# Kernel tuning notes

Hardware: AMD Instinct MI355X
Metric: run time of the kernel (lower is better)

Reference implementation:

```python
import jax, jax.numpy as jnp
import numpy as np

N, E, D, C, G = 100000, 3200000, 128, 10, 512
BN_EPS = 1e-5


def setup_inputs() -> dict:
    key = jax.random.key(0)
    ks = jax.random.split(key, 16)
    s = 0.05
    return {
        "x": jax.random.normal(ks[0], (N, D), jnp.float32),
        "edge_index": jax.random.randint(ks[1], (2, E), 0, N, dtype=jnp.int64),
        "batch": jnp.sort(jax.random.randint(ks[2], (N,), 0, G, dtype=jnp.int64)),
        # 5 stacked GINConv MLPs: Linear->ReLU->Linear->ReLU->BatchNorm
        "conv_W1": jax.random.normal(ks[3], (5, D, D), jnp.float32) * s,
        "conv_b1": jnp.zeros((5, D), jnp.float32),
        "conv_W2": jax.random.normal(ks[4], (5, D, D), jnp.float32) * s,
        "conv_b2": jnp.zeros((5, D), jnp.float32),
        "conv_gamma": jnp.ones((5, D), jnp.float32),
        "conv_beta": jnp.zeros((5, D), jnp.float32),
        # fc1 / fc2: Linear->ReLU->BatchNorm (fc2 is SHARED across stages)
        "fc1_W": jax.random.normal(ks[5], (D, D), jnp.float32) * s,
        "fc1_b": jnp.zeros((D,), jnp.float32),
        "fc1_gamma": jnp.ones((D,), jnp.float32),
        "fc1_beta": jnp.zeros((D,), jnp.float32),
        "fc2_W": jax.random.normal(ks[6], (D, D), jnp.float32) * s,
        "fc2_b": jnp.zeros((D,), jnp.float32),
        "fc2_gamma": jnp.ones((D,), jnp.float32),
        "fc2_beta": jnp.zeros((D,), jnp.float32),
        "lin_W": jax.random.normal(ks[7], (D, C), jnp.float32) * s,
        "lin_b": jnp.zeros((C,), jnp.float32),
    }


def _bn(h, gamma, beta):
    # training-mode BatchNorm1d: batch stats, biased variance
    m = h.mean(axis=0)
    v = h.var(axis=0)
    return (h - m) * jax.lax.rsqrt(v + BN_EPS) * gamma + beta


def _fc(h, W, b, gamma, beta):
    return _bn(jax.nn.relu(h @ W + b), gamma, beta)


def reference(x, edge_index, batch, conv_W1, conv_b1, conv_W2, conv_b2,
              conv_gamma, conv_beta, fc1_W, fc1_b, fc1_gamma, fc1_beta,
              fc2_W, fc2_b, fc2_gamma, fc2_beta, lin_W, lin_b):
    src, dst = edge_index[0], edge_index[1]
    pool = lambda h: jax.ops.segment_sum(h, batch, num_segments=G)

    g = _fc(pool(x), fc1_W, fc1_b, fc1_gamma, fc1_beta)  # x0_g
    total = g
    h = x
    for i in range(5):
        # GINConv, eps=0: nn((1+eps)*x + sum_{j in N(i)} x_j)
        agg = jax.ops.segment_sum(h[src], dst, num_segments=N)
        z = h + agg
        z = jax.nn.relu(z @ conv_W1[i] + conv_b1[i])
        z = jax.nn.relu(z @ conv_W2[i] + conv_b2[i])
        h = _bn(z, conv_gamma[i], conv_beta[i])
        g = _fc(g + pool(h), fc2_W, fc2_b, fc2_gamma, fc2_beta)
        total = total + g
    # dropout omitted (inference); final classifier
    logits = total @ lin_W + lin_b
    return jax.nn.log_softmax(logits, axis=-1)
```

## Files before the change

kernel.cpp:

```cpp
#include <hip/hip_runtime.h>
#include <hip/hip_bf16.h>
#include <math.h>

#define D 128
#define NG 512
#define NC 10
#define PAD 96
#define CAP 704
#define BN_EPS 1e-5f

typedef __attribute__((ext_vector_type(8))) short frag_ab;
typedef __attribute__((ext_vector_type(4))) float f32x4;

__device__ __forceinline__ ushort f2bf(float v) {
    __hip_bfloat16 h = __float2bfloat16(v);
    union { __hip_bfloat16 h; ushort u; } c;
    c.h = h;
    return c.u;
}
__device__ __forceinline__ float bflo(uint u) { return __uint_as_float(u << 16); }
__device__ __forceinline__ float bfhi(uint u) { return __uint_as_float(u & 0xffff0000u); }
__device__ __forceinline__ uint packbf(float x, float y) {
    return (uint)f2bf(x) | ((uint)f2bf(y) << 16);
}

__global__ void zero_ints(int* __restrict__ p, int n) {
    int i = blockIdx.x * blockDim.x + threadIdx.x;
    int s = gridDim.x * blockDim.x;
    for (; i < n; i += s) p[i] = 0;
}

__global__ void scatter_bucket(const int* __restrict__ srcs, const int* __restrict__ dsts, int E,
                               int* __restrict__ bcnt, uint* __restrict__ ebuf) {
    int i = blockIdx.x * blockDim.x + threadIdx.x;
    int s = gridDim.x * blockDim.x;
    for (; i < E; i += s) {
        int d = dsts[i];
        int b = d >> 4;
        int pos = atomicAdd(&bcnt[b], 1);
        if (pos < CAP) ebuf[(size_t)b * CAP + pos] = (uint)srcs[i] | ((uint)(d & 15) << 24);
    }
}

__global__ void csr_phaseB(const uint* __restrict__ ebuf, const int* __restrict__ bcnt,
                           int* __restrict__ cnt, int* __restrict__ pad, int N) {
    int b = blockIdx.x;
    int tid = threadIdx.x;
    int n0 = b << 4;
    __shared__ int lcur[16];
    __shared__ int lcnt2[16];
    __shared__ int lpad[16 * PAD];
    if (tid < 16) lcur[tid] = tid * PAD;
    __syncthreads();
    int ec = bcnt[b];
    if (ec > CAP) ec = CAP;
    const uint* eb = ebuf + (size_t)b * CAP;
    for (int e = tid; e < ec; e += 256) {
        uint w = eb[e];
        int ld = w >> 24;
        int pos = atomicAdd(&lcur[ld], 1);
        if (pos < ld * PAD + PAD) lpad[pos] = (int)(w & 0x00FFFFFFu);
    }
    __syncthreads();
    int ne = N - n0;
    if (ne > 16) ne = 16;
    if (tid < 16) {
        int c = lcur[tid] - tid * PAD;
        if (c > PAD) c = PAD;
        lcnt2[tid] = c;
    }
    __syncthreads();
    if (tid < ne) cnt[n0 + tid] = lcnt2[tid];
    const int CH = PAD / 4;
    int4* dst4 = (int4*)(pad + (size_t)n0 * PAD);
    const int4* s4 = (const int4*)lpad;
    for (int i = tid; i < 16 * CH; i += 256) {
        int node = i / CH, ch = i - node * CH;
        if (node < ne && ch * 4 < lcnt2[node]) dst4[node * CH + ch] = s4[node * CH + ch];
    }
}

__global__ void gstart_bsearch(const int* __restrict__ batch, int N, int* __restrict__ gstart) {
    int g = blockIdx.x * blockDim.x + threadIdx.x;
    if (g > NG) return;
    if (g == NG) { gstart[NG] = N; return; }
    int lo = 0, hi = N;
    while (lo < hi) {
        int mid = (lo + hi) >> 1;
        if (batch[mid] < g) lo = mid + 1; else hi = mid;
    }
    gstart[g] = lo;
}

__global__ void cvt_bf16(const float* __restrict__ in, uint* __restrict__ out, int nPairs) {
    int i = blockIdx.x * blockDim.x + threadIdx.x;
    int s = gridDim.x * blockDim.x;
    const float2* in2 = (const float2*)in;
    for (; i < nPairs; i += s) {
        float2 v = in2[i];
        out[i] = packbf(v.x, v.y);
    }
}

__global__ void prep_w(const float* __restrict__ W1, const float* __restrict__ W2,
                       ushort* __restrict__ Wt) {
    int m = blockIdx.x;
    const float* W = (m < 5) ? (W1 + (size_t)m * D * D) : (W2 + (size_t)(m - 5) * D * D);
    ushort* out = Wt + (size_t)m * D * D;
    __shared__ ushort ws[D * D];
    int tid = threadIdx.x;
    for (int i = tid; i < D * D; i += 256) ws[i] = f2bf(W[i]);
    __syncthreads();
    int n = tid >> 1, kh = (tid & 1) << 6;
    uint* op = (uint*)(out + n * D + kh);
#pragma unroll 8
    for (int j = 0; j < 32; ++j) {
        uint lo = ws[(kh + 2 * j) * D + n];
        uint hi = ws[(kh + 2 * j + 1) * D + n];
        op[j] = lo | (hi << 16);
    }
}

#define ACC8(V) { s0 += bflo(V.x); s1 += bfhi(V.x); s2 += bflo(V.y); s3 += bfhi(V.y); \
                  s4 += bflo(V.z); s5 += bfhi(V.z); s6 += bflo(V.w); s7 += bfhi(V.w); }

__global__ void agg_pad(const uint4* __restrict__ src4, const float* __restrict__ stats,
                        const float* __restrict__ gamma, const float* __restrict__ beta,
                        float invN, const int* __restrict__ deg, const int* __restrict__ pad,
                        uint4* __restrict__ out4, int N) {
    int gtid = blockIdx.x * blockDim.x + threadIdx.x;
    int grp = gtid >> 4;
    int c16 = gtid & 15;
    int ng = (gridDim.x * blockDim.x) >> 4;
    int cb = c16 * 8;
    float A[8], B[8];
#pragma unroll
    for (int j = 0; j < 8; ++j) { A[j] = 1.f; B[j] = 0.f; }
    if (stats) {
#pragma unroll
        for (int j = 0; j < 8; ++j) {
            int c = cb + j;
            float m = stats[c] * invN;
            float v = fmaxf(stats[D + c] * invN - m * m, 0.f);
            float r = rsqrtf(v + BN_EPS);
            A[j] = r * gamma[c];
            B[j] = beta[c] - m * A[j];
        }
    }
    for (int n = grp; n < N; n += ng) {
        float s0 = 0.f, s1 = 0.f, s2 = 0.f, s3 = 0.f, s4 = 0.f, s5 = 0.f, s6 = 0.f, s7 = 0.f;
        {
            uint4 v = src4[(size_t)n * 16 + c16];
            ACC8(v);
        }
        const int* cp = pad + (size_t)n * PAD;
        int dg = deg[n];
        if (dg > PAD) dg = PAD;
        int e = 0;
        for (; e + 8 <= dg; e += 8) {
            int i0 = cp[e], i1 = cp[e + 1], i2 = cp[e + 2], i3 = cp[e + 3];
            int i4 = cp[e + 4], i5 = cp[e + 5], i6 = cp[e + 6], i7 = cp[e + 7];
            uint4 v0 = src4[(size_t)i0 * 16 + c16];
            uint4 v1 = src4[(size_t)i1 * 16 + c16];
            uint4 v2 = src4[(size_t)i2 * 16 + c16];
            uint4 v3 = src4[(size_t)i3 * 16 + c16];
            uint4 v4 = src4[(size_t)i4 * 16 + c16];
            uint4 v5 = src4[(size_t)i5 * 16 + c16];
            uint4 v6 = src4[(size_t)i6 * 16 + c16];
            uint4 v7 = src4[(size_t)i7 * 16 + c16];
            ACC8(v0); ACC8(v1); ACC8(v2); ACC8(v3);
            ACC8(v4); ACC8(v5); ACC8(v6); ACC8(v7);
        }
        for (; e < dg; ++e) {
            uint4 v0 = src4[(size_t)cp[e] * 16 + c16];
            ACC8(v0);
        }
        float db = (float)(dg + 1);
        uint4 o;
        o.x = packbf(s0 * A[0] + db * B[0], s1 * A[1] + db * B[1]);
        o.y = packbf(s2 * A[2] + db * B[2], s3 * A[3] + db * B[3]);
        o.z = packbf(s4 * A[4] + db * B[4], s5 * A[5] + db * B[5]);
        o.w = packbf(s6 * A[6] + db * B[6], s7 * A[7] + db * B[7]);
        out4[(size_t)n * 16 + c16] = o;
    }
}

__launch_bounds__(256, 2)
__global__ void gin_mlp(const uint* __restrict__ z, const ushort* __restrict__ w1t,
                        const float* __restrict__ b1, const ushort* __restrict__ w2t,
                        const float* __restrict__ b2, uint* __restrict__ outp, int N) {
    int tid = threadIdx.x;
    int lane = tid & 63;
    int wv = tid >> 6;
    int col = lane & 15;
    int kq = lane >> 4;
    int blk = blockIdx.x;
    int m0 = blk * 64 + wv * 16;
    __shared__ __align__(16) ushort cs[64 * D];

    int arow = m0 + col;
    if (arow >= N) arow = N - 1;
    const char* zrow = (const char*)z + (size_t)arow * 256 + kq * 16;
    frag_ab a0 = *(const frag_ab*)(zrow);
    frag_ab a1 = *(const frag_ab*)(zrow + 64);
    frag_ab a2 = *(const frag_ab*)(zrow + 128);
    frag_ab a3 = *(const frag_ab*)(zrow + 192);

    f32x4 acc[8];
#pragma unroll
    for (int n = 0; n < 8; ++n) {
        float bz = b1[n * 16 + col];
        acc[n] = (f32x4){bz, bz, bz, bz};
    }
    const char* wl1 = (const char*)w1t + (size_t)col * 256 + kq * 16;
#pragma unroll
    for (int kc = 0; kc < 4; ++kc) {
        frag_ab av = (kc == 0) ? a0 : (kc == 1) ? a1 : (kc == 2) ? a2 : a3;
#pragma unroll
        for (int n = 0; n < 8; ++n) {
            frag_ab bv = *(const frag_ab*)(wl1 + n * 4096 + kc * 64);
            acc[n] = __builtin_amdgcn_mfma_f32_16x16x32_bf16(av, bv, acc[n], 0, 0, 0);
        }
    }
    int rbase = wv * 16 + kq * 4;
#pragma unroll
    for (int n = 0; n < 8; ++n) {
#pragma unroll
        for (int r = 0; r < 4; ++r) {
            int row = rbase + r;
            int colo = n * 16 + col;
            int chunk = (colo >> 3) ^ (row & 15);
            cs[row * D + chunk * 8 + (colo & 7)] = f2bf(fmaxf(acc[n][r], 0.f));
        }
    }
    __syncthreads();

    int lrow = wv * 16 + col;
    frag_ab c0, c1, c2, c3;
    c0 = *(const frag_ab*)(cs + lrow * D + (((0 << 2) + kq) ^ col) * 8);
    c1 = *(const frag_ab*)(cs + lrow * D + (((1 << 2) + kq) ^ col) * 8);
    c2 = *(const frag_ab*)(cs + lrow * D + (((2 << 2) + kq) ^ col) * 8);
    c3 = *(const frag_ab*)(cs + lrow * D + (((3 << 2) + kq) ^ col) * 8);

#pragma unroll
    for (int n = 0; n < 8; ++n) {
        float bz = b2[n * 16 + col];
        acc[n] = (f32x4){bz, bz, bz, bz};
    }
    const char* wl2 = (const char*)w2t + (size_t)col * 256 + kq * 16;
#pragma unroll
    for (int kc = 0; kc < 4; ++kc) {
        frag_ab av = (kc == 0) ? c0 : (kc == 1) ? c1 : (kc == 2) ? c2 : c3;
#pragma unroll
        for (int n = 0; n < 8; ++n) {
            frag_ab bv = *(const frag_ab*)(wl2 + n * 4096 + kc * 64);
            acc[n] = __builtin_amdgcn_mfma_f32_16x16x32_bf16(av, bv, acc[n], 0, 0, 0);
        }
    }
    __syncthreads();

#pragma unroll
    for (int n = 0; n < 8; ++n) {
#pragma unroll
        for (int r = 0; r < 4; ++r) {
            int row = rbase + r;
            int colo = n * 16 + col;
            int chunk = (colo >> 3) ^ (row & 15);
            cs[row * D + chunk * 8 + (colo & 7)] = f2bf(fmaxf(acc[n][r], 0.f));
        }
    }
    __syncthreads();

    const uint4* csv = (const uint4*)cs;
    uint4* og = (uint4*)outp;
#pragma unroll
    for (int p = 0; p < 4; ++p) {
        int idx = p * 256 + tid;
        int row = idx >> 4;
        int j = idx & 15;
        uint4 v = csv[row * 16 + (j ^ (row & 15))];
        if (blk * 64 + row < N) og[(size_t)blk * 1024 + idx] = v;
    }
}

template <int BF16>
__global__ void pool_stats(const void* __restrict__ zptr, const int* __restrict__ gstart,
                           float* __restrict__ pool, float* __restrict__ sq) {
    int g = blockIdx.x;
    int tid = threadIdx.x;
    int r0 = gstart[g], r1 = gstart[g + 1];
    __shared__ float red[256];
    if (BF16) {
        const uint* z = (const uint*)zptr;
        int uc = tid & 63;
        int qq = tid >> 6;
        float s0 = 0.f, s1 = 0.f, q0 = 0.f, q1 = 0.f;
        for (int r = r0 + qq; r < r1; r += 4) {
            uint u = z[(size_t)r * 64 + uc];
            float lo = bflo(u), hi = bfhi(u);
            s0 += lo; s1 += hi;
            q0 += lo * lo; q1 += hi * hi;
        }
        float S0 = 0.f, S1 = 0.f, Q0 = 0.f, Q1 = 0.f;
        red[tid] = s0; __syncthreads();
        if (qq == 0) S0 = red[uc] + red[uc + 64] + red[uc + 128] + red[uc + 192];
        __syncthreads();
        red[tid] = s1; __syncthreads();
        if (qq == 0) S1 = red[uc] + red[uc + 64] + red[uc + 128] + red[uc + 192];
        __syncthreads();
        red[tid] = q0; __syncthreads();
        if (qq == 0) Q0 = red[uc] + red[uc + 64] + red[uc + 128] + red[uc + 192];
        __syncthreads();
        red[tid] = q1; __syncthreads();
        if (qq == 0) Q1 = red[uc] + red[uc + 64] + red[uc + 128] + red[uc + 192];
        if (qq == 0) {
            pool[g * D + 2 * uc] = S0;
            pool[g * D + 2 * uc + 1] = S1;
            sq[g * D + 2 * uc] = Q0;
            sq[g * D + 2 * uc + 1] = Q1;
        }
    } else {
        const float* z = (const float*)zptr;
        int col = tid & 127;
        int half = tid >> 7;
        float s = 0.f;
        for (int r = r0 + half; r < r1; r += 2) s += z[(size_t)r * D + col];
        red[tid] = s;
        __syncthreads();
        if (half == 0) pool[g * D + col] = red[tid] + red[tid + 128];
    }
}

__global__ void col_stats(const float* __restrict__ pool, const float* __restrict__ sq,
                          float* __restrict__ stats) {
    int c = blockIdx.x;
    int tid = threadIdx.x;
    float s = pool[tid * D + c] + pool[(tid + 256) * D + c];
    float q = sq[tid * D + c] + sq[(tid + 256) * D + c];
    __shared__ float rs[256], rq[256];
    rs[tid] = s; rq[tid] = q;
    __syncthreads();
    for (int off = 128; off > 0; off >>= 1) {
        if (tid < off) { rs[tid] += rs[tid + off]; rq[tid] += rq[tid + off]; }
        __syncthreads();
    }
    if (tid == 0) { stats[c] = rs[0]; stats[D + c] = rq[0]; }
}

__global__ void fc_forward(const float* __restrict__ pool, const float* __restrict__ stats,
                           const float* __restrict__ gamma, const float* __restrict__ beta,
                           float invN, const int* __restrict__ gstart, const float* __restrict__ gprev,
                           const float* __restrict__ W, const float* __restrict__ bias,
                           float* __restrict__ y) {
    int g = blockIdx.x;
    int tid = threadIdx.x;
    __shared__ float u[D];
    float pv = pool[g * D + tid];
    float uv;
    if (stats) {
        float m = stats[tid] * invN;
        float var = fmaxf(stats[D + tid] * invN - m * m, 0.f);
        float rs = rsqrtf(var + BN_EPS);
        float a = rs * gamma[tid];
        float b = beta[tid] - m * a;
        float cntg = (float)(gstart[g + 1] - gstart[g]);
        uv = gprev[g * D + tid] + pv * a + cntg * b;
    } else {
        uv = pv;
    }
    u[tid] = uv;
    __syncthreads();
    float acc = bias[tid];
#pragma unroll 8
    for (int k = 0; k < D; ++k) acc = fmaf(u[k], W[k * D + tid], acc);
    y[g * D + tid] = fmaxf(acc, 0.f);
}

__global__ void fc_bn2(const float* __restrict__ y, const float* __restrict__ gamma,
                       const float* __restrict__ beta, float* __restrict__ gbuf,
                       float* __restrict__ total, int first) {
    int col = blockIdx.x;
    int tid = threadIdx.x;
    int i0 = tid * D + col, i1 = (tid + 256) * D + col;
    float v0 = y[i0], v1 = y[i1];
    __shared__ float rs[256], rq[256];
    rs[tid] = v0 + v1;
    rq[tid] = v0 * v0 + v1 * v1;
    __syncthreads();
    for (int off = 128; off > 0; off >>= 1) {
        if (tid < off) { rs[tid] += rs[tid + off]; rq[tid] += rq[tid + off]; }
        __syncthreads();
    }
    __shared__ float ab[2];
    if (tid == 0) {
        const float invG = 1.f / NG;
        float m = rs[0] * invG;
        float var = fmaxf(rq[0] * invG - m * m, 0.f);
        float a = rsqrtf(var + BN_EPS) * gamma[col];
        ab[0] = a;
        ab[1] = beta[col] - m * a;
    }
    __syncthreads();
    float a = ab[0], b = ab[1];
    float g0 = v0 * a + b, g1 = v1 * a + b;
    gbuf[i0] = g0;
    gbuf[i1] = g1;
    if (first) { total[i0] = g0; total[i1] = g1; }
    else { total[i0] += g0; total[i1] += g1; }
}

__global__ void final_logits(const float* __restrict__ total, const float* __restrict__ linW,
                             const float* __restrict__ linb, float* __restrict__ out) {
    int g = blockIdx.x;
    int tid = threadIdx.x;
    __shared__ float t[D];
    __shared__ float lg[12];
    t[tid] = total[g * D + tid];
    __syncthreads();
    if (tid < NC) {
        float a = linb[tid];
        for (int k = 0; k < D; ++k) a = fmaf(t[k], linW[k * NC + tid], a);
        lg[tid] = a;
    }
    __syncthreads();
    if (tid == 0) {
        float mx = lg[0];
        for (int c = 1; c < NC; ++c) mx = fmaxf(mx, lg[c]);
        float se = 0.f;
        for (int c = 0; c < NC; ++c) se += expf(lg[c] - mx);
        lg[10] = mx + logf(se);
    }
    __syncthreads();
    if (tid < NC) out[g * NC + tid] = lg[tid] - lg[10];
}

extern "C" void kernel_launch(void* const* d_in, const int* in_sizes, int n_in,
                              void* d_out, int out_size, void* d_ws, size_t ws_size,
                              hipStream_t stream) {
    const float* x = (const float*)d_in[0];
    const int* edge = (const int*)d_in[1];
    const int* batch = (const int*)d_in[2];
    const float* convW1 = (const float*)d_in[3];
    const float* convb1 = (const float*)d_in[4];
    const float* convW2 = (const float*)d_in[5];
    const float* convb2 = (const float*)d_in[6];
    const float* convgamma = (const float*)d_in[7];
    const float* convbeta = (const float*)d_in[8];
    const float* fc1W = (const float*)d_in[9];
    const float* fc1b = (const float*)d_in[10];
    const float* fc1gamma = (const float*)d_in[11];
    const float* fc1beta = (const float*)d_in[12];
    const float* fc2W = (const float*)d_in[13];
    const float* fc2b = (const float*)d_in[14];
    const float* fc2gamma = (const float*)d_in[15];
    const float* fc2beta = (const float*)d_in[16];
    const float* linW = (const float*)d_in[17];
    const float* linb = (const float*)d_in[18];

    const int N = in_sizes[0] / D;
    const int E = in_sizes[1] / 2;
    const int* srcs = edge;
    const int* dsts = edge + E;
    const float invN = 1.f / (float)N;
    const int NBUK = (N + 15) >> 4;

    char* p = (char*)d_ws;
    auto alloc = [&](size_t bytes) -> void* {
        void* r = (void*)p;
        p += (bytes + 255) & ~(size_t)255;
        return r;
    };
    uint* xb = (uint*)alloc((size_t)N * 64 * 4);
    uint* z  = (uint*)alloc((size_t)N * 64 * 4);
    uint* zB = (uint*)alloc((size_t)N * 64 * 4);
    ushort* wt = (ushort*)alloc((size_t)10 * D * D * 2);
    int* pad = (int*)alloc((size_t)N * PAD * 4);
    int* cnt = (int*)alloc((size_t)N * 4);
    int* gstart = (int*)alloc((size_t)(NG + 1) * 4);
    int* bcnt = (int*)alloc((size_t)NBUK * 4);
    float* stats_all = (float*)alloc((size_t)5 * 2 * D * 4);
    float* pool = (float*)alloc((size_t)NG * D * 4);
    float* sqbuf = (float*)alloc((size_t)NG * D * 4);
    float* ybuf = (float*)alloc((size_t)NG * D * 4);
    float* gbuf = (float*)alloc((size_t)NG * D * 4);
    float* total = (float*)alloc((size_t)NG * D * 4);

    uint* ebuf = z;

    zero_ints<<<(NBUK + 255) / 256, 256, 0, stream>>>(bcnt, NBUK);
    gstart_bsearch<<<3, 256, 0, stream>>>(batch, N, gstart);
    scatter_bucket<<<2048, 256, 0, stream>>>(srcs, dsts, E, bcnt, ebuf);
    cvt_bf16<<<2048, 256, 0, stream>>>(x, xb, N * 64);
    prep_w<<<10, 256, 0, stream>>>(convW1, convW2, wt);
    csr_phaseB<<<NBUK, 256, 0, stream>>>(ebuf, bcnt, cnt, pad, N);

    pool_stats<0><<<NG, 256, 0, stream>>>(x, gstart, pool, nullptr);
    fc_forward<<<NG, D, 0, stream>>>(pool, nullptr, nullptr, nullptr, 0.f, nullptr, nullptr,
                                     fc1W, fc1b, ybuf);
    fc_bn2<<<D, 256, 0, stream>>>(ybuf, fc1gamma, fc1beta, gbuf, total, 1);

    const uint* src = xb;
    const int mlp_grid = (N + 63) / 64;
    for (int i = 0; i < 5; ++i) {
        const float* st = (i == 0) ? nullptr : (stats_all + (size_t)(i - 1) * 2 * D);
        const float* ga = (i == 0) ? nullptr : (convgamma + (size_t)(i - 1) * D);
        const float* be = (i == 0) ? nullptr : (convbeta + (size_t)(i - 1) * D);
        agg_pad<<<2048, 256, 0, stream>>>((const uint4*)src, st, ga, be, invN,
                                          cnt, pad, (uint4*)z, N);
        gin_mlp<<<mlp_grid, 256, 0, stream>>>(z, wt + (size_t)i * D * D, convb1 + (size_t)i * D,
                                              wt + (size_t)(5 + i) * D * D, convb2 + (size_t)i * D,
                                              zB, N);
        float* st_i = stats_all + (size_t)i * 2 * D;
        pool_stats<1><<<NG, 256, 0, stream>>>(zB, gstart, pool, sqbuf);
        col_stats<<<D, 256, 0, stream>>>(pool, sqbuf, st_i);
        fc_forward<<<NG, D, 0, stream>>>(pool, st_i,
                                         convgamma + (size_t)i * D, convbeta + (size_t)i * D,
                                         invN, gstart, gbuf, fc2W, fc2b, ybuf);
        fc_bn2<<<D, 256, 0, stream>>>(ybuf, fc2gamma, fc2beta, gbuf, total, 0);
        src = zB;
    }

    final_logits<<<NG, D, 0, stream>>>(total, linW, linb, (float*)d_out);
}
```

Before: 1.392 ms.

## Fuse neighbor aggregation into GIN MLP kernel via shared-memory tile

The padded-CSR gather-aggregate (with the previous layer's BatchNorm folded in) now runs inside the MLP kernel. Each 64-row block aggregates its rows into a swizzled LDS tile and then feeds it straight to the MFMA stages. This drops the write and re-read of the intermediate z buffer and one kernel launch per layer. Output buffers ping-pong because the source and destination can no longer alias. The cost is a fixed 64-row grid with launch bounds of 2, which may reduce the latency hiding the gather had under the old grid-stride launch.

```diff
diff --git a/kernel.cpp b/kernel.cpp
--- a/kernel.cpp
+++ b/kernel.cpp
@@ -124,87 +124,92 @@
 #define ACC8(V) { s0 += bflo(V.x); s1 += bfhi(V.x); s2 += bflo(V.y); s3 += bfhi(V.y); \
                   s4 += bflo(V.z); s5 += bfhi(V.z); s6 += bflo(V.w); s7 += bfhi(V.w); }
 
-__global__ void agg_pad(const uint4* __restrict__ src4, const float* __restrict__ stats,
-                        const float* __restrict__ gamma, const float* __restrict__ beta,
-                        float invN, const int* __restrict__ deg, const int* __restrict__ pad,
-                        uint4* __restrict__ out4, int N) {
-    int gtid = blockIdx.x * blockDim.x + threadIdx.x;
-    int grp = gtid >> 4;
-    int c16 = gtid & 15;
-    int ng = (gridDim.x * blockDim.x) >> 4;
-    int cb = c16 * 8;
-    float A[8], B[8];
-#pragma unroll
-    for (int j = 0; j < 8; ++j) { A[j] = 1.f; B[j] = 0.f; }
-    if (stats) {
-#pragma unroll
-        for (int j = 0; j < 8; ++j) {
-            int c = cb + j;
-            float m = stats[c] * invN;
-            float v = fmaxf(stats[D + c] * invN - m * m, 0.f);
-            float r = rsqrtf(v + BN_EPS);
-            A[j] = r * gamma[c];
-            B[j] = beta[c] - m * A[j];
-        }
-    }
-    for (int n = grp; n < N; n += ng) {
-        float s0 = 0.f, s1 = 0.f, s2 = 0.f, s3 = 0.f, s4 = 0.f, s5 = 0.f, s6 = 0.f, s7 = 0.f;
-        {
-            uint4 v = src4[(size_t)n * 16 + c16];
-            ACC8(v);
-        }
-        const int* cp = pad + (size_t)n * PAD;
-        int dg = deg[n];
-        if (dg > PAD) dg = PAD;
-        int e = 0;
-        for (; e + 8 <= dg; e += 8) {
-            int i0 = cp[e], i1 = cp[e + 1], i2 = cp[e + 2], i3 = cp[e + 3];
-            int i4 = cp[e + 4], i5 = cp[e + 5], i6 = cp[e + 6], i7 = cp[e + 7];
-            uint4 v0 = src4[(size_t)i0 * 16 + c16];
-            uint4 v1 = src4[(size_t)i1 * 16 + c16];
-            uint4 v2 = src4[(size_t)i2 * 16 + c16];
-            uint4 v3 = src4[(size_t)i3 * 16 + c16];
-            uint4 v4 = src4[(size_t)i4 * 16 + c16];
-            uint4 v5 = src4[(size_t)i5 * 16 + c16];
-            uint4 v6 = src4[(size_t)i6 * 16 + c16];
-            uint4 v7 = src4[(size_t)i7 * 16 + c16];
-            ACC8(v0); ACC8(v1); ACC8(v2); ACC8(v3);
-            ACC8(v4); ACC8(v5); ACC8(v6); ACC8(v7);
-        }
-        for (; e < dg; ++e) {
-            uint4 v0 = src4[(size_t)cp[e] * 16 + c16];
-            ACC8(v0);
-        }
-        float db = (float)(dg + 1);
-        uint4 o;
-        o.x = packbf(s0 * A[0] + db * B[0], s1 * A[1] + db * B[1]);
-        o.y = packbf(s2 * A[2] + db * B[2], s3 * A[3] + db * B[3]);
-        o.z = packbf(s4 * A[4] + db * B[4], s5 * A[5] + db * B[5]);
-        o.w = packbf(s6 * A[6] + db * B[6], s7 * A[7] + db * B[7]);
-        out4[(size_t)n * 16 + c16] = o;
-    }
-}
-
 __launch_bounds__(256, 2)
-__global__ void gin_mlp(const uint* __restrict__ z, const ushort* __restrict__ w1t,
-                        const float* __restrict__ b1, const ushort* __restrict__ w2t,
-                        const float* __restrict__ b2, uint* __restrict__ outp, int N) {
-    int tid = threadIdx.x;
+__global__ void gin_fused(const uint4* __restrict__ src4, const float* __restrict__ stats,
+                          const float* __restrict__ gamma, const float* __restrict__ beta,
+                          float invN, const int* __restrict__ deg, const int* __restrict__ pad,
+                          const ushort* __restrict__ w1t, const float* __restrict__ b1,
+                          const ushort* __restrict__ w2t, const float* __restrict__ b2,
+                          uint* __restrict__ outp, int N) {
+    int tid = threadIdx.x;
+    int blk = blockIdx.x;
+    int m0 = blk * 64;
+    __shared__ __align__(16) uint4 zt4[64 * 16];
+    __shared__ __align__(16) ushort cs[64 * D];
+
+    {
+        int grp = tid >> 4;
+        int c16 = tid & 15;
+        int cb = c16 * 8;
+        float A[8], B[8];
+#pragma unroll
+        for (int j = 0; j < 8; ++j) { A[j] = 1.f; B[j] = 0.f; }
+        if (stats) {
+#pragma unroll
+            for (int j = 0; j < 8; ++j) {
+                int c = cb + j;
+                float m = stats[c] * invN;
+                float v = fmaxf(stats[D + c] * invN - m * m, 0.f);
+                float r = rsqrtf(v + BN_EPS);
+                A[j] = r * gamma[c];
+                B[j] = beta[c] - m * A[j];
+            }
+        }
+#pragma unroll
+        for (int p = 0; p < 4; ++p) {
+            int lr = p * 16 + grp;
+            int n = m0 + lr;
+            uint4 o = {0u, 0u, 0u, 0u};
+            if (n < N) {
+                float s0 = 0.f, s1 = 0.f, s2 = 0.f, s3 = 0.f, s4 = 0.f, s5 = 0.f, s6 = 0.f, s7 = 0.f;
+                {
+                    uint4 v = src4[(size_t)n * 16 + c16];
+                    ACC8(v);
+                }
+                const int* cp = pad + (size_t)n * PAD;
+                int dg = deg[n];
+                if (dg > PAD) dg = PAD;
+                int e = 0;
+                for (; e + 8 <= dg; e += 8) {
+                    int i0 = cp[e], i1 = cp[e + 1], i2 = cp[e + 2], i3 = cp[e + 3];
+                    int i4 = cp[e + 4], i5 = cp[e + 5], i6 = cp[e + 6], i7 = cp[e + 7];
+                    uint4 v0 = src4[(size_t)i0 * 16 + c16];
+                    uint4 v1 = src4[(size_t)i1 * 16 + c16];
+                    uint4 v2 = src4[(size_t)i2 * 16 + c16];
+                    uint4 v3 = src4[(size_t)i3 * 16 + c16];
+                    uint4 v4 = src4[(size_t)i4 * 16 + c16];
+                    uint4 v5 = src4[(size_t)i5 * 16 + c16];
+                    uint4 v6 = src4[(size_t)i6 * 16 + c16];
+                    uint4 v7 = src4[(size_t)i7 * 16 + c16];
+                    ACC8(v0); ACC8(v1); ACC8(v2); ACC8(v3);
+                    ACC8(v4); ACC8(v5); ACC8(v6); ACC8(v7);
+                }
+                for (; e < dg; ++e) {
+                    uint4 v0 = src4[(size_t)cp[e] * 16 + c16];
+                    ACC8(v0);
+                }
+                float db = (float)(dg + 1);
+                o.x = packbf(s0 * A[0] + db * B[0], s1 * A[1] + db * B[1]);
+                o.y = packbf(s2 * A[2] + db * B[2], s3 * A[3] + db * B[3]);
+                o.z = packbf(s4 * A[4] + db * B[4], s5 * A[5] + db * B[5]);
+                o.w = packbf(s6 * A[6] + db * B[6], s7 * A[7] + db * B[7]);
+            }
+            zt4[lr * 16 + (c16 ^ (lr & 15))] = o;
+        }
+    }
+    __syncthreads();
+
     int lane = tid & 63;
     int wv = tid >> 6;
     int col = lane & 15;
     int kq = lane >> 4;
-    int blk = blockIdx.x;
-    int m0 = blk * 64 + wv * 16;
-    __shared__ __align__(16) ushort cs[64 * D];
-
-    int arow = m0 + col;
-    if (arow >= N) arow = N - 1;
-    const char* zrow = (const char*)z + (size_t)arow * 256 + kq * 16;
-    frag_ab a0 = *(const frag_ab*)(zrow);
-    frag_ab a1 = *(const frag_ab*)(zrow + 64);
-    frag_ab a2 = *(const frag_ab*)(zrow + 128);
-    frag_ab a3 = *(const frag_ab*)(zrow + 192);
+    int lrow = wv * 16 + col;
+    const ushort* ztc = (const ushort*)zt4;
+
+    frag_ab a0 = *(const frag_ab*)(ztc + lrow * D + (((0 << 2) + kq) ^ col) * 8);
+    frag_ab a1 = *(const frag_ab*)(ztc + lrow * D + (((1 << 2) + kq) ^ col) * 8);
+    frag_ab a2 = *(const frag_ab*)(ztc + lrow * D + (((2 << 2) + kq) ^ col) * 8);
+    frag_ab a3 = *(const frag_ab*)(ztc + lrow * D + (((3 << 2) + kq) ^ col) * 8);
 
     f32x4 acc[8];
 #pragma unroll
@@ -235,12 +240,10 @@
     }
     __syncthreads();
 
-    int lrow = wv * 16 + col;
-    frag_ab c0, c1, c2, c3;
-    c0 = *(const frag_ab*)(cs + lrow * D + (((0 << 2) + kq) ^ col) * 8);
-    c1 = *(const frag_ab*)(cs + lrow * D + (((1 << 2) + kq) ^ col) * 8);
-    c2 = *(const frag_ab*)(cs + lrow * D + (((2 << 2) + kq) ^ col) * 8);
-    c3 = *(const frag_ab*)(cs + lrow * D + (((3 << 2) + kq) ^ col) * 8);
+    frag_ab c0 = *(const frag_ab*)(cs + lrow * D + (((0 << 2) + kq) ^ col) * 8);
+    frag_ab c1 = *(const frag_ab*)(cs + lrow * D + (((1 << 2) + kq) ^ col) * 8);
+    frag_ab c2 = *(const frag_ab*)(cs + lrow * D + (((2 << 2) + kq) ^ col) * 8);
+    frag_ab c3 = *(const frag_ab*)(cs + lrow * D + (((3 << 2) + kq) ^ col) * 8);
 
 #pragma unroll
     for (int n = 0; n < 8; ++n) {
@@ -279,7 +282,7 @@
         int row = idx >> 4;
         int j = idx & 15;
         uint4 v = csv[row * 16 + (j ^ (row & 15))];
-        if (blk * 64 + row < N) og[(size_t)blk * 1024 + idx] = v;
+        if (m0 + row < N) og[(size_t)blk * 1024 + idx] = v;
     }
 }
 
@@ -471,7 +474,7 @@
         return r;
     };
     uint* xb = (uint*)alloc((size_t)N * 64 * 4);
-    uint* z  = (uint*)alloc((size_t)N * 64 * 4);
+    uint* zA = (uint*)alloc((size_t)N * 64 * 4);
     uint* zB = (uint*)alloc((size_t)N * 64 * 4);
     ushort* wt = (ushort*)alloc((size_t)10 * D * D * 2);
     int* pad = (int*)alloc((size_t)N * PAD * 4);
@@ -485,7 +488,7 @@
     float* gbuf = (float*)alloc((size_t)NG * D * 4);
     float* total = (float*)alloc((size_t)NG * D * 4);
 
-    uint* ebuf = z;
+    uint* ebuf = zB;
 
     zero_ints<<<(NBUK + 255) / 256, 256, 0, stream>>>(bcnt, NBUK);
     gstart_bsearch<<<3, 256, 0, stream>>>(batch, N, gstart);
@@ -500,24 +503,25 @@
     fc_bn2<<<D, 256, 0, stream>>>(ybuf, fc1gamma, fc1beta, gbuf, total, 1);
 
     const uint* src = xb;
-    const int mlp_grid = (N + 63) / 64;
+    uint* dst = zA;
+    const int fgrid = (N + 63) / 64;
     for (int i = 0; i < 5; ++i) {
         const float* st = (i == 0) ? nullptr : (stats_all + (size_t)(i - 1) * 2 * D);
         const float* ga = (i == 0) ? nullptr : (convgamma + (size_t)(i - 1) * D);
         const float* be = (i == 0) ? nullptr : (convbeta + (size_t)(i - 1) * D);
-        agg_pad<<<2048, 256, 0, stream>>>((const uint4*)src, st, ga, be, invN,
-                                          cnt, pad, (uint4*)z, N);
-        gin_mlp<<<mlp_grid, 256, 0, stream>>>(z, wt + (size_t)i * D * D, convb1 + (size_t)i * D,
-                                              wt + (size_t)(5 + i) * D * D, convb2 + (size_t)i * D,
-                                              zB, N);
+        gin_fused<<<fgrid, 256, 0, stream>>>((const uint4*)src, st, ga, be, invN, cnt, pad,
+                                             wt + (size_t)i * D * D, convb1 + (size_t)i * D,
+                                             wt + (size_t)(5 + i) * D * D, convb2 + (size_t)i * D,
+                                             dst, N);
         float* st_i = stats_all + (size_t)i * 2 * D;
-        pool_stats<1><<<NG, 256, 0, stream>>>(zB, gstart, pool, sqbuf);
+        pool_stats<1><<<NG, 256, 0, stream>>>(dst, gstart, pool, sqbuf);
         col_stats<<<D, 256, 0, stream>>>(pool, sqbuf, st_i);
         fc_forward<<<NG, D, 0, stream>>>(pool, st_i,
                                          convgamma + (size_t)i * D, convbeta + (size_t)i * D,
                                          invN, gstart, gbuf, fc2W, fc2b, ybuf);
         fc_bn2<<<D, 256, 0, stream>>>(ybuf, fc2gamma, fc2beta, gbuf, total, 0);
-        src = zB;
+        src = dst;
+        dst = (dst == zA) ? zB : zA;
     }
 
     final_logits<<<NG, D, 0, stream>>>(total, linW, linb, (float*)d_out);
```

New measurement: 1.429 ms. 1.03x slower.
